# Performance work log

Hardware: AMD Instinct MI355X
Metric: run time of the kernel (lower is better)

## Reference

```python
import jax, jax.numpy as jnp
import numpy as np

N_NODES = 50000
N_EDGES = 800000
D_FEAT = 128
HIDDEN = 256
N_CLASSES = 2


def setup_inputs() -> dict:
    key = jax.random.key(0)
    ks = jax.random.split(key, 9)
    x = jax.random.normal(ks[0], (N_NODES, D_FEAT), dtype=jnp.float32)
    edge_index = jax.random.randint(ks[1], (2, N_EDGES), 0, N_NODES, dtype=jnp.int32)
    # SAGEConv params: lin_l (applied to aggregated neighbors), lin_r (root), bias
    s1 = 1.0 / np.sqrt(D_FEAT)
    s2 = 1.0 / np.sqrt(HIDDEN)
    W1l = jax.random.normal(ks[2], (D_FEAT, HIDDEN), dtype=jnp.float32) * s1
    W1r = jax.random.normal(ks[3], (D_FEAT, HIDDEN), dtype=jnp.float32) * s1
    b1 = jax.random.normal(ks[4], (HIDDEN,), dtype=jnp.float32) * s1
    W2l = jax.random.normal(ks[5], (HIDDEN, N_CLASSES), dtype=jnp.float32) * s2
    W2r = jax.random.normal(ks[6], (HIDDEN, N_CLASSES), dtype=jnp.float32) * s2
    b2 = jax.random.normal(ks[7], (N_CLASSES,), dtype=jnp.float32) * s2
    return {"x": x, "edge_index": edge_index, "W1l": W1l, "W1r": W1r,
            "b1": b1, "W2l": W2l, "W2r": W2r, "b2": b2}


def _sage_conv(x, src, dst, Wl, Wr, b):
    # mean-aggregate neighbor features x[src] into destination nodes
    n = x.shape[0]
    agg = jax.ops.segment_sum(x[src], dst, num_segments=n)  # [N, d]
    deg = jax.ops.segment_sum(jnp.ones((src.shape[0],), x.dtype), dst,
                              num_segments=n)
    mean = agg / jnp.maximum(deg, 1.0)[:, None]
    return mean @ Wl + x @ Wr + b


def reference(x, edge_index, W1l, W1r, b1, W2l, W2r, b2):
    src, dst = edge_index[0], edge_index[1]
    h = jax.nn.relu(_sage_conv(x, src, dst, W1l, W1r, b1))
    embeddings = h  # dropout is identity in eval mode
    out = jax.nn.sigmoid(_sage_conv(embeddings, src, dst, W2l, W2r, b2))
    return out, embeddings
```

## Files before the change

kernel.cpp:

```cpp
#include <hip/hip_runtime.h>
#include <math.h>

#define N_NODES 50000
#define N_EDGES 800000
#define D_FEAT 128
#define HIDDEN 256
#define NB_SCAN 196
#define NB_CVT 12500
#define NB_CNT 3125
#define NB_WF 256
#define GEMM_BLOCKS 782

typedef __bf16 bf16x8 __attribute__((ext_vector_type(8)));
typedef float f32x4 __attribute__((ext_vector_type(4)));

__device__ __forceinline__ unsigned short f2b(float f) {
    unsigned u = __builtin_bit_cast(unsigned, f);
    return (unsigned short)((u + 0x7fff + ((u >> 16) & 1)) >> 16);
}

__global__ __launch_bounds__(256) void prep(
    const float* __restrict__ x, const int* __restrict__ dst,
    const float* __restrict__ W1l, const float* __restrict__ W1r,
    unsigned* __restrict__ Arow, int* __restrict__ cnt,
    unsigned short* __restrict__ Wfrag) {
    int b = blockIdx.x;
    if (b < NB_CVT) {
        int t = b * 256 + threadIdx.x;
        float2 v = *(const float2*)(x + (size_t)t * 2);
        int d = t >> 6, j = t & 63;
        Arow[(size_t)d * 128 + 64 + j] = (unsigned)f2b(v.x) | ((unsigned)f2b(v.y) << 16);
    } else if (b < NB_CVT + NB_CNT) {
        int e = (b - NB_CVT) * 256 + threadIdx.x;
        atomicAdd(&cnt[dst[e]], 1);
    } else {
        int t = (b - NB_CVT - NB_CNT) * 256 + threadIdx.x;
        int j = t & 7;
        int lane = (t >> 3) & 63;
        int ks = (t >> 9) & 7;
        int nt = t >> 12;
        int k = ks * 32 + ((lane >> 4) << 3) + j;
        int n = (nt << 4) + (lane & 15);
        float v = (k < 128) ? W1l[k * 256 + n] : W1r[(k - 128) * 256 + n];
        Wfrag[t] = f2b(v);
    }
}

__global__ void scan1(const int* __restrict__ cnt, int* __restrict__ bsum) {
    __shared__ int tmp[256];
    int t = threadIdx.x;
    int i = blockIdx.x * 256 + t;
    tmp[t] = (i < N_NODES) ? cnt[i] : 0;
    __syncthreads();
    for (int off = 128; off > 0; off >>= 1) {
        if (t < off) tmp[t] += tmp[t + off];
        __syncthreads();
    }
    if (t == 0) bsum[blockIdx.x] = tmp[0];
}

__global__ void scan2(const int* __restrict__ bsum, int* __restrict__ boff) {
    __shared__ int tmp[256];
    int t = threadIdx.x;
    int v = (t < NB_SCAN) ? bsum[t] : 0;
    tmp[t] = v;
    __syncthreads();
    for (int off = 1; off < 256; off <<= 1) {
        int y = (t >= off) ? tmp[t - off] : 0;
        __syncthreads();
        tmp[t] += y;
        __syncthreads();
    }
    if (t < NB_SCAN) boff[t] = tmp[t] - v;
}

__global__ void scan3(const int* __restrict__ cnt, const int* __restrict__ boff,
                      int* __restrict__ rowpos) {
    __shared__ int tmp[256];
    int t = threadIdx.x;
    int i = blockIdx.x * 256 + t;
    int v = (i < N_NODES) ? cnt[i] : 0;
    tmp[t] = v;
    __syncthreads();
    for (int off = 1; off < 256; off <<= 1) {
        int y = (t >= off) ? tmp[t - off] : 0;
        __syncthreads();
        tmp[t] += y;
        __syncthreads();
    }
    if (i < N_NODES) rowpos[i] = tmp[t] - v + boff[blockIdx.x];
}

__global__ void fill_kernel(const int* __restrict__ src, const int* __restrict__ dst,
                            int* __restrict__ rowpos, unsigned short* __restrict__ esrc) {
    int e = blockIdx.x * blockDim.x + threadIdx.x;
    if (e < N_EDGES) {
        int pos = atomicAdd(&rowpos[dst[e]], 1);
        esrc[pos] = (unsigned short)src[e];
    }
}

__global__ __launch_bounds__(256) void agg1(
    const unsigned* __restrict__ Arow_x, unsigned* __restrict__ Arow_m,
    const unsigned short* __restrict__ esrc,
    const int* __restrict__ rowend, const int* __restrict__ cnt) {
    int d = blockIdx.x * 4 + (threadIdx.x >> 6);
    int lane = threadIdx.x & 63;
    int end = rowend[d];
    int c = cnt[d];
    float a0 = 0.0f, a1 = 0.0f;
    for (int base = end - c; base < end; base += 64) {
        int m = end - base; if (m > 64) m = 64;
        int idx = base + lane;
        int e = (int)esrc[idx < end ? idx : end - 1];
        for (int j0 = 0; j0 < m; j0 += 8) {
#pragma unroll
            for (int j = 0; j < 8; j++) {
                int s = __shfl(e, j0 + j);
                unsigned u = Arow_x[(size_t)s * 128 + 64 + lane];
                float sc = (j0 + j < m) ? 1.0f : 0.0f;
                a0 += sc * __builtin_bit_cast(float, u << 16);
                a1 += sc * __builtin_bit_cast(float, u & 0xffff0000u);
            }
        }
    }
    float inv = 1.0f / fmaxf((float)c, 1.0f);
    unsigned lo = (unsigned)f2b(a0 * inv);
    unsigned hi = (unsigned)f2b(a1 * inv);
    Arow_m[(size_t)d * 128 + lane] = lo | (hi << 16);
}

__global__ __launch_bounds__(256) void gemm1ps(
    const unsigned* __restrict__ Arow, const unsigned short* __restrict__ Wfrag,
    const float* __restrict__ b1, const float* __restrict__ W2l,
    const float* __restrict__ W2r, const float* __restrict__ b2,
    float* __restrict__ h, float* __restrict__ p, float* __restrict__ s) {
    __shared__ unsigned A[64 * 128];
    __shared__ float ppart[64][4];

    int r0 = blockIdx.x * 64;
    int tid = threadIdx.x;
    int w = tid >> 6;
    int lane = tid & 63;
    int quad = lane >> 4;
    int l15 = lane & 15;

    ((float*)ppart)[tid] = 0.0f;

    int sr = tid >> 2;
    int cb = (tid & 3) << 3;
#pragma unroll
    for (int j = 0; j < 8; j++) {
        int c = cb + j;
        uint4 v = *(const uint4*)(Arow + (size_t)(r0 + sr) * 128 + (c << 2));
        int cp = c ^ (sr & 7);
        *(uint4*)(A + sr * 128 + (cp << 2)) = v;
    }
    __syncthreads();

    f32x4 acc[16];
#pragma unroll
    for (int i = 0; i < 16; i++) acc[i] = (f32x4){0.0f, 0.0f, 0.0f, 0.0f};

    for (int ks = 0; ks < 8; ks++) {
        bf16x8 bfr[4];
#pragma unroll
        for (int nt = 0; nt < 4; nt++) {
            int ntg = (w << 2) + nt;
            uint4 raw = *(const uint4*)(Wfrag + ((((ntg << 3) + ks) << 6) + lane) * 8);
            bfr[nt] = __builtin_bit_cast(bf16x8, raw);
        }
#pragma unroll
        for (int mt = 0; mt < 4; mt++) {
            int row = (mt << 4) + l15;
            int c = (ks << 2) + quad;
            uint4 araw = *(const uint4*)(A + row * 128 + ((c ^ (row & 7)) << 2));
            bf16x8 afr = __builtin_bit_cast(bf16x8, araw);
#pragma unroll
            for (int nt = 0; nt < 4; nt++) {
                acc[(mt << 2) + nt] = __builtin_amdgcn_mfma_f32_16x16x32_bf16(
                    afr, bfr[nt], acc[(mt << 2) + nt], 0, 0, 0);
            }
        }
    }

    float w2[4][4];
#pragma unroll
    for (int nt = 0; nt < 4; nt++) {
        int col = (w << 6) + (nt << 4) + l15;
        float2 l2 = *(const float2*)(W2l + col * 2);
        float2 r2 = *(const float2*)(W2r + col * 2);
        w2[nt][0] = l2.x; w2[nt][1] = l2.y; w2[nt][2] = r2.x; w2[nt][3] = r2.y;
    }

#pragma unroll
    for (int mt = 0; mt < 4; mt++) {
        float red[4][4];
#pragma unroll
        for (int v = 0; v < 4; v++)
#pragma unroll
            for (int r = 0; r < 4; r++) red[v][r] = 0.0f;

#pragma unroll
        for (int nt = 0; nt < 4; nt++) {
            int col = (w << 6) + (nt << 4) + l15;
            float b = b1[col];
            f32x4 v = acc[(mt << 2) + nt];
#pragma unroll
            for (int r = 0; r < 4; r++) {
                float hv = v[r] + b;
                hv = hv > 0.0f ? hv : 0.0f;
                int row = r0 + (mt << 4) + (quad << 2) + r;
                if (row < N_NODES) h[(size_t)row * 256 + col] = hv;
                red[0][r] += hv * w2[nt][0];
                red[1][r] += hv * w2[nt][1];
                red[2][r] += hv * w2[nt][2];
                red[3][r] += hv * w2[nt][3];
            }
        }
#pragma unroll
        for (int v = 0; v < 4; v++)
#pragma unroll
            for (int r = 0; r < 4; r++) {
                red[v][r] += __shfl_xor(red[v][r], 1);
                red[v][r] += __shfl_xor(red[v][r], 2);
                red[v][r] += __shfl_xor(red[v][r], 4);
                red[v][r] += __shfl_xor(red[v][r], 8);
            }
        if (l15 == 0) {
            int lrow = (mt << 4) + (quad << 2);
#pragma unroll
            for (int r = 0; r < 4; r++)
#pragma unroll
                for (int v = 0; v < 4; v++)
                    atomicAdd(&ppart[lrow + r][v], red[v][r]);
        }
    }
    __syncthreads();

    if (tid < 64) {
        int row = r0 + tid;
        if (row < N_NODES) {
            float2 pv = {ppart[tid][0], ppart[tid][1]};
            float2 sv = {ppart[tid][2] + b2[0], ppart[tid][3] + b2[1]};
            *(float2*)(p + (size_t)row * 2) = pv;
            *(float2*)(s + (size_t)row * 2) = sv;
        }
    }
}

__global__ __launch_bounds__(256) void agg2(
    const float* __restrict__ p, const float* __restrict__ s,
    const unsigned short* __restrict__ esrc,
    const int* __restrict__ rowend, const int* __restrict__ cnt,
    float* __restrict__ out) {
    int d = blockIdx.x * 4 + (threadIdx.x >> 6);
    int lane = threadIdx.x & 63;
    int end = rowend[d];
    int c = cnt[d];
    float a0 = 0.0f, a1 = 0.0f;
    for (int base = end - c; base < end; base += 64) {
        int idx = base + lane;
        if (idx < end) {
            int ss = (int)esrc[idx];
            float2 v = *(const float2*)(p + (size_t)ss * 2);
            a0 += v.x; a1 += v.y;
        }
    }
#pragma unroll
    for (int off = 32; off > 0; off >>= 1) {
        a0 += __shfl_down(a0, off);
        a1 += __shfl_down(a1, off);
    }
    if (lane == 0) {
        float inv = 1.0f / fmaxf((float)c, 1.0f);
        float z0 = a0 * inv + s[(size_t)d * 2 + 0];
        float z1 = a1 * inv + s[(size_t)d * 2 + 1];
        float2 o = {1.0f / (1.0f + expf(-z0)), 1.0f / (1.0f + expf(-z1))};
        *(float2*)(out + (size_t)d * 2) = o;
    }
}

extern "C" void kernel_launch(void* const* d_in, const int* in_sizes, int n_in,
                              void* d_out, int out_size, void* d_ws, size_t ws_size,
                              hipStream_t stream) {
    const float* x   = (const float*)d_in[0];
    const int*   ei  = (const int*)d_in[1];
    const float* W1l = (const float*)d_in[2];
    const float* W1r = (const float*)d_in[3];
    const float* b1  = (const float*)d_in[4];
    const float* W2l = (const float*)d_in[5];
    const float* W2r = (const float*)d_in[6];
    const float* b2  = (const float*)d_in[7];

    const int* src = ei;
    const int* dst = ei + N_EDGES;

    float* out = (float*)d_out;
    float* emb = out + (size_t)N_NODES * 2;

    int* cnt    = (int*)d_ws;
    int* rowpos = cnt + N_NODES;
    int* bsum   = rowpos + N_NODES;
    int* boff   = bsum + 256;
    unsigned short* esrc = (unsigned short*)(boff + 256);
    unsigned* Arow = (unsigned*)(esrc + 800064);
    unsigned short* Wfrag = (unsigned short*)(Arow + (size_t)50048 * 128);
    float* p = (float*)(Wfrag + 65536);
    float* s = p + (size_t)N_NODES * 2;

    hipMemsetAsync(cnt, 0, N_NODES * sizeof(int), stream);

    prep<<<NB_CVT + NB_CNT + NB_WF, 256, 0, stream>>>(x, dst, W1l, W1r, Arow, cnt, Wfrag);

    scan1<<<NB_SCAN, 256, 0, stream>>>(cnt, bsum);
    scan2<<<1, 256, 0, stream>>>(bsum, boff);
    scan3<<<NB_SCAN, 256, 0, stream>>>(cnt, boff, rowpos);
    fill_kernel<<<NB_CNT, 256, 0, stream>>>(src, dst, rowpos, esrc);

    agg1<<<N_NODES / 4, 256, 0, stream>>>(Arow, Arow, esrc, rowpos, cnt);

    gemm1ps<<<GEMM_BLOCKS, 256, 0, stream>>>(Arow, Wfrag, b1, W2l, W2r, b2, emb, p, s);

    agg2<<<N_NODES / 4, 256, 0, stream>>>(p, s, esrc, rowpos, cnt, out);
}
```

Baseline: 258.4 us.

## Use grid-stride loops, vectorize x conversion, merge scan passes

Several kernels (prep, fill, agg1, agg2) now launch a fixed, smaller grid and use grid-stride loops instead of one block per work item. The x-to-bf16 conversion moves from float2 to two float4 loads with a uint4 store. The second and third scan kernels are merged into one, with each block redoing the 196-element block-sum scan in shared memory. The aim is to cut launch count and block scheduling overhead. The cost is redundant scan work and possibly less latency hiding in the gather-heavy aggregation kernels.

```diff
diff --git a/kernel.cpp b/kernel.cpp
--- a/kernel.cpp
+++ b/kernel.cpp
@@ -6,17 +6,20 @@
 #define D_FEAT 128
 #define HIDDEN 256
 #define NB_SCAN 196
-#define NB_CVT 12500
-#define NB_CNT 3125
-#define NB_WF 256
 #define GEMM_BLOCKS 782
+
+#define PREP_CVT_B 512
+#define PREP_CNT_B 256
+#define PREP_WF_B 64
+#define FILL_B 512
+#define AGG_B 2048
 
 typedef __bf16 bf16x8 __attribute__((ext_vector_type(8)));
 typedef float f32x4 __attribute__((ext_vector_type(4)));
 
-__device__ __forceinline__ unsigned short f2b(float f) {
+__device__ __forceinline__ unsigned f2b(float f) {
     unsigned u = __builtin_bit_cast(unsigned, f);
-    return (unsigned short)((u + 0x7fff + ((u >> 16) & 1)) >> 16);
+    return (u + 0x7fff + ((u >> 16) & 1)) >> 16;
 }
 
 __global__ __launch_bounds__(256) void prep(
@@ -25,24 +28,35 @@
     unsigned* __restrict__ Arow, int* __restrict__ cnt,
     unsigned short* __restrict__ Wfrag) {
     int b = blockIdx.x;
-    if (b < NB_CVT) {
-        int t = b * 256 + threadIdx.x;
-        float2 v = *(const float2*)(x + (size_t)t * 2);
-        int d = t >> 6, j = t & 63;
-        Arow[(size_t)d * 128 + 64 + j] = (unsigned)f2b(v.x) | ((unsigned)f2b(v.y) << 16);
-    } else if (b < NB_CVT + NB_CNT) {
-        int e = (b - NB_CVT) * 256 + threadIdx.x;
-        atomicAdd(&cnt[dst[e]], 1);
+    int t = threadIdx.x;
+    if (b < PREP_CVT_B) {
+        for (int g = b * 256 + t; g < 800000; g += PREP_CVT_B * 256) {
+            float4 v0 = *(const float4*)(x + (size_t)g * 8);
+            float4 v1 = *(const float4*)(x + (size_t)g * 8 + 4);
+            uint4 o;
+            o.x = f2b(v0.x) | (f2b(v0.y) << 16);
+            o.y = f2b(v0.z) | (f2b(v0.w) << 16);
+            o.z = f2b(v1.x) | (f2b(v1.y) << 16);
+            o.w = f2b(v1.z) | (f2b(v1.w) << 16);
+            int d = g >> 4;
+            int j = (g << 2) & 63;
+            *(uint4*)(Arow + (size_t)d * 128 + 64 + j) = o;
+        }
+    } else if (b < PREP_CVT_B + PREP_CNT_B) {
+        for (int e = (b - PREP_CVT_B) * 256 + t; e < N_EDGES; e += PREP_CNT_B * 256)
+            atomicAdd(&cnt[dst[e]], 1);
     } else {
-        int t = (b - NB_CVT - NB_CNT) * 256 + threadIdx.x;
-        int j = t & 7;
-        int lane = (t >> 3) & 63;
-        int ks = (t >> 9) & 7;
-        int nt = t >> 12;
-        int k = ks * 32 + ((lane >> 4) << 3) + j;
-        int n = (nt << 4) + (lane & 15);
-        float v = (k < 128) ? W1l[k * 256 + n] : W1r[(k - 128) * 256 + n];
-        Wfrag[t] = f2b(v);
+        for (int tt = (b - PREP_CVT_B - PREP_CNT_B) * 256 + t; tt < 65536;
+             tt += PREP_WF_B * 256) {
+            int j = tt & 7;
+            int lane = (tt >> 3) & 63;
+            int ks = (tt >> 9) & 7;
+            int nt = tt >> 12;
+            int k = ks * 32 + ((lane >> 4) << 3) + j;
+            int n = (nt << 4) + (lane & 15);
+            float v = (k < 128) ? W1l[k * 256 + n] : W1r[(k - 128) * 256 + n];
+            Wfrag[tt] = (unsigned short)f2b(v);
+        }
     }
 }
 
@@ -59,10 +73,23 @@
     if (t == 0) bsum[blockIdx.x] = tmp[0];
 }
 
-__global__ void scan2(const int* __restrict__ bsum, int* __restrict__ boff) {
+__global__ void scanB(const int* __restrict__ cnt, const int* __restrict__ bsum,
+                      int* __restrict__ rowpos) {
+    __shared__ int bs[256];
     __shared__ int tmp[256];
     int t = threadIdx.x;
-    int v = (t < NB_SCAN) ? bsum[t] : 0;
+    int b = blockIdx.x;
+    bs[t] = (t < NB_SCAN) ? bsum[t] : 0;
+    __syncthreads();
+    for (int off = 1; off < 256; off <<= 1) {
+        int y = (t >= off) ? bs[t - off] : 0;
+        __syncthreads();
+        bs[t] += y;
+        __syncthreads();
+    }
+    int boff = (b == 0) ? 0 : bs[b - 1];
+    int i = b * 256 + t;
+    int v = (i < N_NODES) ? cnt[i] : 0;
     tmp[t] = v;
     __syncthreads();
     for (int off = 1; off < 256; off <<= 1) {
@@ -71,30 +98,13 @@
         tmp[t] += y;
         __syncthreads();
     }
-    if (t < NB_SCAN) boff[t] = tmp[t] - v;
-}
-
-__global__ void scan3(const int* __restrict__ cnt, const int* __restrict__ boff,
-                      int* __restrict__ rowpos) {
-    __shared__ int tmp[256];
-    int t = threadIdx.x;
-    int i = blockIdx.x * 256 + t;
-    int v = (i < N_NODES) ? cnt[i] : 0;
-    tmp[t] = v;
-    __syncthreads();
-    for (int off = 1; off < 256; off <<= 1) {
-        int y = (t >= off) ? tmp[t - off] : 0;
-        __syncthreads();
-        tmp[t] += y;
-        __syncthreads();
-    }
-    if (i < N_NODES) rowpos[i] = tmp[t] - v + boff[blockIdx.x];
-}
-
-__global__ void fill_kernel(const int* __restrict__ src, const int* __restrict__ dst,
-                            int* __restrict__ rowpos, unsigned short* __restrict__ esrc) {
-    int e = blockIdx.x * blockDim.x + threadIdx.x;
-    if (e < N_EDGES) {
+    if (i < N_NODES) rowpos[i] = tmp[t] - v + boff;
+}
+
+__global__ __launch_bounds__(256) void fill_kernel(
+    const int* __restrict__ src, const int* __restrict__ dst,
+    int* __restrict__ rowpos, unsigned short* __restrict__ esrc) {
+    for (int e = blockIdx.x * 256 + threadIdx.x; e < N_EDGES; e += FILL_B * 256) {
         int pos = atomicAdd(&rowpos[dst[e]], 1);
         esrc[pos] = (unsigned short)src[e];
     }
@@ -104,30 +114,30 @@
     const unsigned* __restrict__ Arow_x, unsigned* __restrict__ Arow_m,
     const unsigned short* __restrict__ esrc,
     const int* __restrict__ rowend, const int* __restrict__ cnt) {
-    int d = blockIdx.x * 4 + (threadIdx.x >> 6);
+    int wid = (blockIdx.x * 256 + threadIdx.x) >> 6;
     int lane = threadIdx.x & 63;
-    int end = rowend[d];
-    int c = cnt[d];
-    float a0 = 0.0f, a1 = 0.0f;
-    for (int base = end - c; base < end; base += 64) {
-        int m = end - base; if (m > 64) m = 64;
-        int idx = base + lane;
-        int e = (int)esrc[idx < end ? idx : end - 1];
-        for (int j0 = 0; j0 < m; j0 += 8) {
-#pragma unroll
-            for (int j = 0; j < 8; j++) {
-                int s = __shfl(e, j0 + j);
-                unsigned u = Arow_x[(size_t)s * 128 + 64 + lane];
-                float sc = (j0 + j < m) ? 1.0f : 0.0f;
-                a0 += sc * __builtin_bit_cast(float, u << 16);
-                a1 += sc * __builtin_bit_cast(float, u & 0xffff0000u);
-            }
-        }
-    }
-    float inv = 1.0f / fmaxf((float)c, 1.0f);
-    unsigned lo = (unsigned)f2b(a0 * inv);
-    unsigned hi = (unsigned)f2b(a1 * inv);
-    Arow_m[(size_t)d * 128 + lane] = lo | (hi << 16);
+    for (int d = wid; d < N_NODES; d += AGG_B * 4) {
+        int end = rowend[d];
+        int c = cnt[d];
+        float a0 = 0.0f, a1 = 0.0f;
+        for (int base = end - c; base < end; base += 64) {
+            int m = end - base; if (m > 64) m = 64;
+            int idx = base + lane;
+            int e = (int)esrc[idx < end ? idx : end - 1];
+            for (int j0 = 0; j0 < m; j0 += 8) {
+#pragma unroll
+                for (int j = 0; j < 8; j++) {
+                    int s = __shfl(e, j0 + j);
+                    unsigned u = Arow_x[(size_t)s * 128 + 64 + lane];
+                    float sc = (j0 + j < m) ? 1.0f : 0.0f;
+                    a0 += sc * __builtin_bit_cast(float, u << 16);
+                    a1 += sc * __builtin_bit_cast(float, u & 0xffff0000u);
+                }
+            }
+        }
+        float inv = 1.0f / fmaxf((float)c, 1.0f);
+        Arow_m[(size_t)d * 128 + lane] = f2b(a0 * inv) | (f2b(a1 * inv) << 16);
+    }
 }
 
 __global__ __launch_bounds__(256) void gemm1ps(
@@ -254,30 +264,32 @@
     const unsigned short* __restrict__ esrc,
     const int* __restrict__ rowend, const int* __restrict__ cnt,
     float* __restrict__ out) {
-    int d = blockIdx.x * 4 + (threadIdx.x >> 6);
+    int wid = (blockIdx.x * 256 + threadIdx.x) >> 6;
     int lane = threadIdx.x & 63;
-    int end = rowend[d];
-    int c = cnt[d];
-    float a0 = 0.0f, a1 = 0.0f;
-    for (int base = end - c; base < end; base += 64) {
-        int idx = base + lane;
-        if (idx < end) {
-            int ss = (int)esrc[idx];
-            float2 v = *(const float2*)(p + (size_t)ss * 2);
-            a0 += v.x; a1 += v.y;
-        }
-    }
-#pragma unroll
-    for (int off = 32; off > 0; off >>= 1) {
-        a0 += __shfl_down(a0, off);
-        a1 += __shfl_down(a1, off);
-    }
-    if (lane == 0) {
-        float inv = 1.0f / fmaxf((float)c, 1.0f);
-        float z0 = a0 * inv + s[(size_t)d * 2 + 0];
-        float z1 = a1 * inv + s[(size_t)d * 2 + 1];
-        float2 o = {1.0f / (1.0f + expf(-z0)), 1.0f / (1.0f + expf(-z1))};
-        *(float2*)(out + (size_t)d * 2) = o;
+    for (int d = wid; d < N_NODES; d += AGG_B * 4) {
+        int end = rowend[d];
+        int c = cnt[d];
+        float a0 = 0.0f, a1 = 0.0f;
+        for (int base = end - c; base < end; base += 64) {
+            int idx = base + lane;
+            if (idx < end) {
+                int ss = (int)esrc[idx];
+                float2 v = *(const float2*)(p + (size_t)ss * 2);
+                a0 += v.x; a1 += v.y;
+            }
+        }
+#pragma unroll
+        for (int off = 32; off > 0; off >>= 1) {
+            a0 += __shfl_down(a0, off);
+            a1 += __shfl_down(a1, off);
+        }
+        if (lane == 0) {
+            float inv = 1.0f / fmaxf((float)c, 1.0f);
+            float z0 = a0 * inv + s[(size_t)d * 2 + 0];
+            float z1 = a1 * inv + s[(size_t)d * 2 + 1];
+            float2 o = {1.0f / (1.0f + expf(-z0)), 1.0f / (1.0f + expf(-z1))};
+            *(float2*)(out + (size_t)d * 2) = o;
+        }
     }
 }
 
@@ -302,8 +314,7 @@
     int* cnt    = (int*)d_ws;
     int* rowpos = cnt + N_NODES;
     int* bsum   = rowpos + N_NODES;
-    int* boff   = bsum + 256;
-    unsigned short* esrc = (unsigned short*)(boff + 256);
+    unsigned short* esrc = (unsigned short*)(bsum + 256);
     unsigned* Arow = (unsigned*)(esrc + 800064);
     unsigned short* Wfrag = (unsigned short*)(Arow + (size_t)50048 * 128);
     float* p = (float*)(Wfrag + 65536);
@@ -311,16 +322,16 @@
 
     hipMemsetAsync(cnt, 0, N_NODES * sizeof(int), stream);
 
-    prep<<<NB_CVT + NB_CNT + NB_WF, 256, 0, stream>>>(x, dst, W1l, W1r, Arow, cnt, Wfrag);
+    prep<<<PREP_CVT_B + PREP_CNT_B + PREP_WF_B, 256, 0, stream>>>(
+        x, dst, W1l, W1r, Arow, cnt, Wfrag);
 
     scan1<<<NB_SCAN, 256, 0, stream>>>(cnt, bsum);
-    scan2<<<1, 256, 0, stream>>>(bsum, boff);
-    scan3<<<NB_SCAN, 256, 0, stream>>>(cnt, boff, rowpos);
-    fill_kernel<<<NB_CNT, 256, 0, stream>>>(src, dst, rowpos, esrc);
-
-    agg1<<<N_NODES / 4, 256, 0, stream>>>(Arow, Arow, esrc, rowpos, cnt);
+    scanB<<<NB_SCAN, 256, 0, stream>>>(cnt, bsum, rowpos);
+    fill_kernel<<<FILL_B, 256, 0, stream>>>(src, dst, rowpos, esrc);
+
+    agg1<<<AGG_B, 256, 0, stream>>>(Arow, Arow, esrc, rowpos, cnt);
 
     gemm1ps<<<GEMM_BLOCKS, 256, 0, stream>>>(Arow, Wfrag, b1, W2l, W2r, b2, emb, p, s);
 
-    agg2<<<N_NODES / 4, 256, 0, stream>>>(p, s, esrc, rowpos, cnt, out);
-}
+    agg2<<<AGG_B, 256, 0, stream>>>(p, s, esrc, rowpos, cnt, out);
+}
```

Measured after the change: 260.0 us. About the same (+0.6%).
